# Kernel optimization log

Hardware: AMD Instinct MI355X
Metric: run time of the kernel (lower is better)

Reference implementation:

```python
import jax, jax.numpy as jnp
import numpy as np

# __init__ constants
COORS_RANGE = ((-51.2, 51.2), (-51.2, 51.2), (-4.0, 2.4))  # x, y, z ranges
SPATIAL = (512, 512, 64)  # base spatial shape (X, Y, Z)
SCALES = (2, 4, 8, 1)     # scale_list + [1]
N_POINTS = 2_000_000
N_BATCH = 8


def setup_inputs() -> dict:
    key = jax.random.key(0)
    kp, kb = jax.random.split(key)
    lo = jnp.array([r[0] for r in COORS_RANGE], dtype=jnp.float32)
    hi = jnp.array([r[1] for r in COORS_RANGE], dtype=jnp.float32)
    u = jax.random.uniform(kp, (N_POINTS, 3), dtype=jnp.float32)
    points = lo + u * (hi - lo)  # [N,3] xyz inside the voxelization range
    batch_idx = jax.random.randint(kb, (N_POINTS,), 0, N_BATCH).astype(jnp.int64)
    return {"points": points, "batch_idx": batch_idx}


def reference(points, batch_idx):
    """Per scale: quantize xyz to voxel indices, then unique/dedup with inverse and
    counts. Rows [b,x,y,z] are packed into a single int64 key so that a 1-D unique
    (lexicographically equivalent to torch.unique(dim=0)) can be used.
    Returns, for each scale in SCALES: (full_coors [N,4] int64, coors_inv [N] int,
    coors [M,4] int32 in [b,z,y,x] order), flattened into one tuple."""
    b = batch_idx.astype(jnp.int64)
    outs = []
    for scale in SCALES:
        dims = [int(np.ceil(s / scale)) for s in SPATIAL]  # per-scale grid size
        idxs = []
        for i in range(3):
            lo, hi = COORS_RANGE[i]
            # torch .long() truncates toward zero; values are >=0 in range so
            # truncation == floor here.
            idxs.append((dims[i] * (points[:, i] - lo) / (hi - lo)).astype(jnp.int64))
        xidx, yidx, zidx = idxs
        full_coors = jnp.stack([b, xidx, yidx, zidx], axis=-1)  # [N,4]
        sx, sy, sz = dims
        # pack (b,x,y,z) lexicographically into one key
        keys = ((b * sx + xidx) * sy + yidx) * sz + zidx
        unq, unq_inv, unq_cnt = jnp.unique(keys, return_inverse=True, return_counts=True)
        zb = unq % sz
        rem = unq // sz
        yb = rem % sy
        rem = rem // sy
        xb = rem % sx
        bb = rem // sx
        # original reorders unq columns to [b, z, y, x] and casts to int32
        coors = jnp.stack([bb, zb, yb, xb], axis=-1).astype(jnp.int32)
        outs.extend([full_coors, unq_inv.reshape(-1), coors])
    return tuple(outs)
```

## Files before the change

### kernel.cpp

```cpp
#include <hip/hip_runtime.h>
#include <stdint.h>


#define CHUNK 4096
#define NB    1174
#define TOTALW 4808704
#define R_S2 0
#define R_S4 528384
#define R_S8 598016
#define R_S1 610304
#define PAD0 524288
#define PAD1 593920
#define PAD2 606208
#define PAD3 4804608
#define NBUCKET 512
#define BCAP 5120
#define KEYBLOCKS 1024
#define ROUND 2048
#define KPT 8
#define NB_SMALL 149

__device__ __forceinline__ uint32_t cmp2(uint32_t w) {
  w = (w | (w >> 1)) & 0x55555555u;
  w = (w | (w >> 1)) & 0x33333333u;
  w = (w | (w >> 2)) & 0x0F0F0F0Fu;
  w = (w | (w >> 4)) & 0x00FF00FFu;
  w = (w | (w >> 8)) & 0x0000FFFFu;
  return w;
}

__global__ __launch_bounds__(256) void k_key(
    const float* __restrict__ pts, const int* __restrict__ bidx, int n,
    uint32_t* __restrict__ keys,
    uint32_t* __restrict__ bucketCount, uint32_t* __restrict__ bucketData,
    uint32_t* __restrict__ chunkSums) {
  __shared__ uint32_t cnt[NBUCKET], inc[NBUCKET], pos[NBUCKET], gpos[NBUCKET];
  __shared__ uint32_t shs[256];
  __shared__ uint32_t scratch[ROUND];
  int t = threadIdx.x;
  int base = blockIdx.x * ROUND;

  if (blockIdx.x == 0) {
    if (t < 149) chunkSums[t] = 0;
    if (t == 149) chunkSums[1173] = 0;
  }

  cnt[t] = 0; cnt[t + 256] = 0;
  pos[t] = 0; pos[t + 256] = 0;
  __syncthreads();

  uint32_t myKey[KPT];
  int myBk[KPT];
#pragma unroll
  for (int k = 0; k < KPT; k++) {
    int j = base + k * 256 + t;
    myBk[k] = -1;
    if (j < n) {
      float px = pts[3 * j + 0];
      float py = pts[3 * j + 1];
      float pz = pts[3 * j + 2];
      int b = bidx[j];
      int x1 = (int)((512.0f * (px + 51.2f)) / 102.4f);
      int y1 = (int)((512.0f * (py + 51.2f)) / 102.4f);
      int z1 = (int)((64.0f * (pz + 4.0f)) / 6.4f);
      keys[j] = ((uint32_t)b << 27) | ((uint32_t)x1 << 17) | ((uint32_t)y1 << 7) | (uint32_t)z1;
      uint32_t s1k = (uint32_t)(((b * 512 + x1) * 512 + y1) * 64 + z1);
      if (s1k < (1u << 27)) {
        int bk = (int)(s1k >> 18);
        myBk[k] = bk;
        myKey[k] = s1k;
        atomicAdd(&cnt[bk], 1u);
      }
    }
  }
  __syncthreads();

  uint32_t c0 = cnt[2 * t], c1 = cnt[2 * t + 1];
  gpos[2 * t] = c0 ? atomicAdd(&bucketCount[2 * t], c0) : 0u;
  gpos[2 * t + 1] = c1 ? atomicAdd(&bucketCount[2 * t + 1], c1) : 0u;
  uint32_t s = c0 + c1;
  shs[t] = s;
  __syncthreads();
  for (int off = 1; off < 256; off <<= 1) {
    uint32_t add = (t >= off) ? shs[t - off] : 0u;
    __syncthreads();
    shs[t] += add;
    __syncthreads();
  }
  inc[2 * t] = shs[t] - s + c0;
  inc[2 * t + 1] = shs[t];
  __syncthreads();
  uint32_t total = shs[255];

#pragma unroll
  for (int k = 0; k < KPT; k++) {
    if (myBk[k] >= 0) {
      int bk = myBk[k];
      uint32_t slot = inc[bk] - cnt[bk] + atomicAdd(&pos[bk], 1u);
      scratch[slot] = myKey[k];
    }
  }
  __syncthreads();

#pragma unroll
  for (int m = 0; m < KPT; m++) {
    uint32_t p = (uint32_t)(m * 256 + t);
    if (p < total) {
      uint32_t kk = scratch[p];
      int lo = (int)(kk >> 18);
      uint32_t lidx = p - (inc[lo] - cnt[lo]);
      uint32_t g = gpos[lo] + lidx;
      if (g < BCAP) bucketData[(size_t)lo * BCAP + g] = kk;
    }
  }
}

__device__ __forceinline__ uint32_t blockReduce(uint32_t v, uint32_t* shR, int t) {
  shR[t] = v;
  __syncthreads();
  for (int off = 128; off > 0; off >>= 1) {
    if (t < off) shR[t] += shR[t + off];
    __syncthreads();
  }
  uint32_t r = shR[0];
  __syncthreads();
  return r;
}

__global__ __launch_bounds__(256) void k_bucket(
    const uint32_t* __restrict__ bucketCount, const uint32_t* __restrict__ bucketData,
    uint32_t* __restrict__ bitmap, uint32_t* __restrict__ chunkSums,
    uint2* __restrict__ pairs) {
  __shared__ uint32_t s1L[8192];
  __shared__ uint32_t s2L[1024];
  __shared__ uint32_t s4L[128];
  __shared__ uint32_t shR[256];
  int bk = blockIdx.x, t = threadIdx.x;

  uint4 z4 = make_uint4(0, 0, 0, 0);
  for (int i = t; i < 2048; i += 256) ((uint4*)s1L)[i] = z4;

  if (bk < 3) {
    const int pads[3] = {PAD0, PAD1, PAD2};
    uint4* pz = (uint4*)(bitmap + pads[bk]);
    for (int i = t; i < 1024; i += 256) pz[i] = z4;
  } else if (bk == 3) {
    uint4* pz = (uint4*)(pairs + PAD3);
    for (int i = t; i < 2048; i += 256) pz[i] = z4;
  }
  __syncthreads();

  uint32_t c = bucketCount[bk];
  if (c > BCAP) c = BCAP;
  const uint32_t* src = bucketData + (size_t)bk * BCAP;
  for (uint32_t i = t; i < c; i += 256) {
    uint32_t key = src[i];
    uint32_t local = key & 0x3FFFFu;
    atomicOr(&s1L[local >> 5], 1u << (local & 31u));
  }
  __syncthreads();

  uint32_t wsum = 0;
#pragma unroll
  for (int m = 0; m < 8; m++) {
    uint4 v = ((uint4*)s1L)[8 * t + m];
    wsum += __popc(v.x) + __popc(v.y) + __popc(v.z) + __popc(v.w);
  }
  shR[t] = wsum;
  __syncthreads();
  for (int off = 1; off < 256; off <<= 1) {
    uint32_t add = (t >= off) ? shR[t - off] : 0u;
    __syncthreads();
    shR[t] += add;
    __syncthreads();
  }
  uint32_t S1a = shR[127];
  uint32_t S1b = shR[255] - S1a;
  uint32_t run = shR[t] - wsum;
  if (t >= 128) run -= S1a;
  __syncthreads();
  {
    uint4* pb = (uint4*)(pairs + (R_S1 + (size_t)bk * 8192));
#pragma unroll
    for (int m = 0; m < 8; m++) {
      uint4 v = ((uint4*)s1L)[8 * t + m];
      uint32_t r0 = run;               uint32_t p0 = __popc(v.x);
      uint32_t r1 = r0 + p0;           uint32_t p1 = __popc(v.y);
      uint32_t r2 = r1 + p1;           uint32_t p2 = __popc(v.z);
      uint32_t r3 = r2 + p2;           run = r3 + __popc(v.w);
      int q = (32 * t + 4 * m) >> 1;
      pb[q + 0] = make_uint4(v.x, r0, v.y, r1);
      pb[q + 1] = make_uint4(v.z, r2, v.w, r3);
    }
  }

  for (int i = t; i < 1024; i += 256) {
    int x2r = i >> 8, Y2 = i & 255;
    int a = (2 * x2r * 512 + 2 * Y2) * 2;
    int b2 = ((2 * x2r + 1) * 512 + 2 * Y2) * 2;
    uint32_t Ax = s1L[a], Ay = s1L[a + 1], Az = s1L[a + 2], Aw = s1L[a + 3];
    uint32_t Bx = s1L[b2], By = s1L[b2 + 1], Bz = s1L[b2 + 2], Bw = s1L[b2 + 3];
    s2L[i] = cmp2(Ax | Az | Bx | Bz) | (cmp2(Ay | Aw | By | Bw) << 16);
  }
  __syncthreads();
  uint32_t pc2 = 0;
  for (int i = t; i < 1024; i += 256) {
    uint32_t v = s2L[i];
    bitmap[R_S2 + (size_t)bk * 1024 + i] = v;
    pc2 += __popc(v);
  }

  uint32_t pc4 = 0;
  if (t < 128) {
    int x4r = t >> 6, kk = t & 63;
    int a = (2 * x4r) * 256 + 4 * kk;
    int b4 = (2 * x4r + 1) * 256 + 4 * kk;
    uint32_t A0 = s2L[a], A1 = s2L[a + 1], A2 = s2L[a + 2], A3 = s2L[a + 3];
    uint32_t B0 = s2L[b4], B1 = s2L[b4 + 1], B2 = s2L[b4 + 2], B3 = s2L[b4 + 3];
    uint32_t v = cmp2(A0 | A1 | B0 | B1) | (cmp2(A2 | A3 | B2 | B3) << 16);
    s4L[t] = v;
    pc4 = __popc(v);
  }
  __syncthreads();
  if (t < 128) bitmap[R_S4 + (size_t)bk * 128 + t] = s4L[t];

  uint32_t pc8 = 0;
  if (t < 16) {
    uint32_t res = 0;
#pragma unroll
    for (int j = 0; j < 4; j++) {
      uint32_t u = s4L[4 * t + j] | s4L[64 + 4 * t + j];
      u = (u | (u >> 16)) & 0xFFFFu;
      res |= cmp2(u) << (8 * j);
    }
    bitmap[R_S8 + (size_t)bk * 16 + t] = res;
    pc8 = __popc(res);
  }

  uint32_t S2 = blockReduce(pc2, shR, t);
  uint32_t S4 = blockReduce(pc4, shR, t);
  uint32_t S8 = blockReduce(pc8, shR, t);
  if (t == 0) {
    chunkSums[149 + 2 * bk] = S1a;
    chunkSums[150 + 2 * bk] = S1b;
    atomicAdd(&chunkSums[bk >> 2], S2);
    atomicAdd(&chunkSums[129 + (bk >> 5)], S4);
    atomicAdd(&chunkSums[146 + (bk >> 8)], S8);
  }
}

__global__ __launch_bounds__(256) void k_scanB(
    uint32_t* blockSums, long long* devOff, uint32_t* devRank, long long fiveN) {
  __shared__ uint32_t sh[256];
  __shared__ uint32_t shB[3];
  int t = threadIdx.x;
  uint32_t v[8];
  uint32_t s = 0;
#pragma unroll
  for (int k = 0; k < 8; k++) {
    int idx = t * 8 + k;
    uint32_t x = (idx < NB) ? blockSums[idx] : 0u;
    v[k] = x;
    s += x;
  }
  sh[t] = s;
  __syncthreads();
  for (int off = 1; off < 256; off <<= 1) {
    uint32_t add = (t >= off) ? sh[t - off] : 0u;
    __syncthreads();
    sh[t] += add;
    __syncthreads();
  }
  uint32_t run = sh[t] - s;
#pragma unroll
  for (int k = 0; k < 8; k++) {
    int idx = t * 8 + k;
    if (idx < NB) blockSums[idx] = run;
    if (idx == 129) shB[0] = run;
    if (idx == 146) shB[1] = run;
    if (idx == 149) shB[2] = run;
    run += v[k];
  }
  __syncthreads();
  if (t == 0) {
    uint32_t tot = sh[255];
    uint32_t T0 = shB[0];
    uint32_t T1 = shB[1] - shB[0];
    uint32_t T2 = shB[2] - shB[1];
    uint32_t T3 = tot - shB[2];
    devOff[0] = 0;
    devOff[1] = devOff[0] + fiveN + 4LL * T0;
    devOff[2] = devOff[1] + fiveN + 4LL * T1;
    devOff[3] = devOff[2] + fiveN + 4LL * T2;
    devOff[4] = devOff[3] + fiveN + 4LL * T3;
    devRank[0] = 0;
    devRank[1] = shB[0];
    devRank[2] = shB[1];
    devRank[3] = shB[2];
  }
}

__global__ __launch_bounds__(256) void k_pref(
    const uint32_t* __restrict__ bitmap, const uint32_t* __restrict__ blockSums,
    uint2* __restrict__ pairs) {
  __shared__ uint32_t sh[256];
  int t = threadIdx.x;
  size_t w0 = (size_t)blockIdx.x * CHUNK + t * 16;
  const uint4* bp = (const uint4*)(bitmap + w0);
  uint4 words[4];
  uint32_t s = 0;
#pragma unroll
  for (int k = 0; k < 4; k++) {
    uint4 v = bp[k];
    words[k] = v;
    s += __popc(v.x) + __popc(v.y) + __popc(v.z) + __popc(v.w);
  }
  sh[t] = s;
  __syncthreads();
  for (int off = 1; off < 256; off <<= 1) {
    uint32_t add = (t >= off) ? sh[t - off] : 0u;
    __syncthreads();
    sh[t] += add;
    __syncthreads();
  }
  uint32_t run = blockSums[blockIdx.x] + (sh[t] - s);
  uint4* pp = (uint4*)(pairs + w0);
#pragma unroll
  for (int k = 0; k < 4; k++) {
    uint4 o1, o2;
    o1.x = words[k].x; o1.y = run; run += __popc(words[k].x);
    o1.z = words[k].y; o1.w = run; run += __popc(words[k].y);
    o2.x = words[k].z; o2.y = run; run += __popc(words[k].z);
    o2.z = words[k].w; o2.w = run; run += __popc(words[k].w);
    pp[2 * k] = o1;
    pp[2 * k + 1] = o2;
  }
}

template <int LZ, int LYZ, int LB, int MZ, int MY, int MX, int RG, int SCALE_IDX>
__device__ __forceinline__ void uniq_region(
    uint32_t w, uint32_t wd, uint32_t pf, uint32_t rankBase,
    const long long* __restrict__ devOff, int* __restrict__ out, long long fiveN) {
  uint32_t pos = pf - rankBase;
  long long base = devOff[SCALE_IDX] + fiveN;
  uint32_t local = w - (uint32_t)RG;
  while (wd) {
    int bit = __ffs(wd) - 1;
    wd &= wd - 1u;
    uint32_t key = (local << 5) + (uint32_t)bit;
    int z = (int)(key & (uint32_t)MZ);
    int y = (int)((key >> LZ) & (uint32_t)MY);
    int x = (int)((key >> LYZ) & (uint32_t)MX);
    int bb = (int)(key >> LB);
    *(int4*)(out + base + 4LL * pos) = make_int4(bb, z, y, x);
    pos++;
  }
}

__global__ __launch_bounds__(256) void k_out(
    const uint32_t* __restrict__ keys, int n, const uint2* __restrict__ pairs,
    const uint32_t* __restrict__ devRank, const long long* __restrict__ devOff,
    const uint32_t* __restrict__ cs, int* __restrict__ out,
    long long fourN, long long fiveN, int NW) {
  int bid = blockIdx.x;
  int t = threadIdx.x;
  if (bid < 4 * NW) {
    int sec = bid / NW;
    int wb = bid - sec * NW;
    if (sec == 0) {
      long long o = devOff[3];
      uint32_t rnk = devRank[3];
#pragma unroll
      for (int half = 0; half < 2; half++) {
        int j = wb * 512 + half * 256 + t;
        if (j >= n) continue;
        uint32_t p = keys[j];
        int b = (int)(p >> 27);
        int x1 = (int)((p >> 17) & 1023u);
        int y1 = (int)((p >> 7) & 1023u);
        int z1 = (int)(p & 127u);
        uint32_t key = (uint32_t)(((b * 512 + x1) * 512 + y1) * 64 + z1);
        uint2 pr = pairs[R_S1 + (key >> 5)];
        *(int4*)(out + o + 4LL * j) = make_int4(b, x1, y1, z1);
        uint32_t inv = cs[149 + (key >> 17)] + pr.y +
                       __popc(pr.x & ((1u << (key & 31u)) - 1u)) - rnk;
        out[o + fourN + j] = (int)inv;
      }
    } else {
      int i = sec - 1;
      const int SX[3] = {256, 128, 64};
      const int SZ[3] = {32, 16, 8};
      const int SH[3] = {1, 2, 3};
      const int RG[3] = {R_S2, R_S4, R_S8};
      int sh = SH[i], sx = SX[i], sz = SZ[i], rg = RG[i];
      long long o = devOff[i];
      uint32_t rnk = devRank[i];
#pragma unroll
      for (int half = 0; half < 2; half++) {
        int j = wb * 512 + half * 256 + t;
        if (j >= n) continue;
        uint32_t p = keys[j];
        int b = (int)(p >> 27);
        int x1 = (int)((p >> 17) & 1023u);
        int y1 = (int)((p >> 7) & 1023u);
        int z1 = (int)(p & 127u);
        int xi = x1 >> sh, yi = y1 >> sh, zi = z1 >> sh;
        uint32_t key = (uint32_t)(((b * sx + xi) * sx + yi) * sz + zi);
        uint2 pr = pairs[rg + (key >> 5)];
        *(int4*)(out + o + 4LL * j) = make_int4(b, xi, yi, zi);
        uint32_t inv = pr.y + __popc(pr.x & ((1u << (key & 31u)) - 1u)) - rnk;
        out[o + fourN + j] = (int)inv;
      }
    }
  } else {
    uint32_t w = (uint32_t)(bid - 4 * NW) * 256 + t;
    uint2 pr = pairs[w];
    if (!pr.x) return;
    if (w < R_S4) {
      uniq_region<5, 13, 21, 31, 255, 255, R_S2, 0>(w, pr.x, pr.y, devRank[0], devOff, out, fiveN);
    } else if (w < R_S8) {
      uniq_region<4, 11, 18, 15, 127, 127, R_S4, 1>(w, pr.x, pr.y, devRank[1], devOff, out, fiveN);
    } else if (w < R_S1) {
      uniq_region<3, 9, 15, 7, 63, 63, R_S8, 2>(w, pr.x, pr.y, devRank[2], devOff, out, fiveN);
    } else {
      uniq_region<6, 15, 24, 63, 511, 511, R_S1, 3>(
          w, pr.x, pr.y + cs[w >> 12], devRank[3], devOff, out, fiveN);
    }
  }
}

extern "C" void kernel_launch(void* const* d_in, const int* in_sizes, int n_in,
                              void* d_out, int out_size, void* d_ws, size_t ws_size,
                              hipStream_t stream) {
  const float* pts = (const float*)d_in[0];
  const int* bidx = (const int*)d_in[1];
  int n = in_sizes[0] / 3;
  int* out = (int*)d_out;

  char* ws = (char*)d_ws;
  long long* devOff = (long long*)ws;
  uint32_t* devRank = (uint32_t*)(ws + 64);
  uint32_t* chunkSums = (uint32_t*)(ws + 256);
  uint32_t* bucketCount = (uint32_t*)(ws + 5120);
  uint32_t* bitmap = (uint32_t*)(ws + 8192);
  uint2* pairs = (uint2*)(ws + 19243008);
  uint32_t* keys = (uint32_t*)(ws + 57712640);
  uint32_t* bucketData = (uint32_t*)(ws + 65712640);

  const long long fourN = 4LL * n, fiveN = 5LL * n;
  const int NW = (n + 511) / 512;

  hipMemsetAsync(bucketCount, 0, NBUCKET * 4, stream);
  hipLaunchKernelGGL(k_key, dim3(KEYBLOCKS), dim3(256), 0, stream,
                     pts, bidx, n, keys, bucketCount, bucketData, chunkSums);
  hipLaunchKernelGGL(k_bucket, dim3(NBUCKET), dim3(256), 0, stream,
                     bucketCount, bucketData, bitmap, chunkSums, pairs);
  hipLaunchKernelGGL(k_scanB, dim3(1), dim3(256), 0, stream, chunkSums, devOff, devRank, fiveN);
  hipLaunchKernelGGL(k_pref, dim3(NB_SMALL), dim3(256), 0, stream, bitmap, chunkSums, pairs);
  hipLaunchKernelGGL(k_out, dim3(4 * NW + TOTALW / 256), dim3(256), 0, stream,
                     keys, n, pairs, devRank, devOff, chunkSums, out, fourN, fiveN, NW);
}
```

Measured before the change: 427.4 us.

## Fuse coarse-scale prefix computation into bucket kernel and drop k_pref pass

The bucket kernel now computes per-bucket exclusive prefix counts for the 2x, 4x and 8x coarse bitmaps and writes (word, prefix) pairs directly. The separate bitmap buffer and the k_pref kernel go away, and a single-block scan produces per-bucket bases that k_out adds on lookup. This removes one kernel launch plus a bitmap write and re-read. In exchange, k_bucket runs extra block-wide scans with many syncthreads, and k_out does one more global load per inverse index.

Result: no change. 422.6 us (median of 2 runs) (-1.1%).

```diff
diff --git a/kernel.cpp b/kernel.cpp
--- a/kernel.cpp
+++ b/kernel.cpp
@@ -2,8 +2,6 @@
 #include <stdint.h>
 
 
-#define CHUNK 4096
-#define NB    1174
 #define TOTALW 4808704
 #define R_S2 0
 #define R_S4 528384
@@ -15,10 +13,10 @@
 #define PAD3 4804608
 #define NBUCKET 512
 #define BCAP 5120
+#define NSUM 2560
 #define KEYBLOCKS 1024
 #define ROUND 2048
 #define KPT 8
-#define NB_SMALL 149
 
 __device__ __forceinline__ uint32_t cmp2(uint32_t w) {
   w = (w | (w >> 1)) & 0x55555555u;
@@ -29,21 +27,28 @@
   return w;
 }
 
+__device__ __forceinline__ uint32_t scan256(uint32_t v, uint32_t* shR, int t) {
+  __syncthreads();
+  shR[t] = v;
+  __syncthreads();
+  for (int off = 1; off < 256; off <<= 1) {
+    uint32_t add = (t >= off) ? shR[t - off] : 0u;
+    __syncthreads();
+    shR[t] += add;
+    __syncthreads();
+  }
+  return shR[t];
+}
+
 __global__ __launch_bounds__(256) void k_key(
     const float* __restrict__ pts, const int* __restrict__ bidx, int n,
     uint32_t* __restrict__ keys,
-    uint32_t* __restrict__ bucketCount, uint32_t* __restrict__ bucketData,
-    uint32_t* __restrict__ chunkSums) {
+    uint32_t* __restrict__ bucketCount, uint32_t* __restrict__ bucketData) {
   __shared__ uint32_t cnt[NBUCKET], inc[NBUCKET], pos[NBUCKET], gpos[NBUCKET];
   __shared__ uint32_t shs[256];
   __shared__ uint32_t scratch[ROUND];
   int t = threadIdx.x;
   int base = blockIdx.x * ROUND;
-
-  if (blockIdx.x == 0) {
-    if (t < 149) chunkSums[t] = 0;
-    if (t == 149) chunkSums[1173] = 0;
-  }
 
   cnt[t] = 0; cnt[t + 256] = 0;
   pos[t] = 0; pos[t + 256] = 0;
@@ -115,22 +120,9 @@
   }
 }
 
-__device__ __forceinline__ uint32_t blockReduce(uint32_t v, uint32_t* shR, int t) {
-  shR[t] = v;
-  __syncthreads();
-  for (int off = 128; off > 0; off >>= 1) {
-    if (t < off) shR[t] += shR[t + off];
-    __syncthreads();
-  }
-  uint32_t r = shR[0];
-  __syncthreads();
-  return r;
-}
-
 __global__ __launch_bounds__(256) void k_bucket(
     const uint32_t* __restrict__ bucketCount, const uint32_t* __restrict__ bucketData,
-    uint32_t* __restrict__ bitmap, uint32_t* __restrict__ chunkSums,
-    uint2* __restrict__ pairs) {
+    uint32_t* __restrict__ sums, uint2* __restrict__ pairs) {
   __shared__ uint32_t s1L[8192];
   __shared__ uint32_t s2L[1024];
   __shared__ uint32_t s4L[128];
@@ -140,12 +132,9 @@
   uint4 z4 = make_uint4(0, 0, 0, 0);
   for (int i = t; i < 2048; i += 256) ((uint4*)s1L)[i] = z4;
 
-  if (bk < 3) {
-    const int pads[3] = {PAD0, PAD1, PAD2};
-    uint4* pz = (uint4*)(bitmap + pads[bk]);
-    for (int i = t; i < 1024; i += 256) pz[i] = z4;
-  } else if (bk == 3) {
-    uint4* pz = (uint4*)(pairs + PAD3);
+  if (bk < 4) {
+    const int pads[4] = {PAD0, PAD1, PAD2, PAD3};
+    uint4* pz = (uint4*)(pairs + pads[bk]);
     for (int i = t; i < 2048; i += 256) pz[i] = z4;
   }
   __syncthreads();
@@ -166,19 +155,11 @@
     uint4 v = ((uint4*)s1L)[8 * t + m];
     wsum += __popc(v.x) + __popc(v.y) + __popc(v.z) + __popc(v.w);
   }
-  shR[t] = wsum;
-  __syncthreads();
-  for (int off = 1; off < 256; off <<= 1) {
-    uint32_t add = (t >= off) ? shR[t - off] : 0u;
-    __syncthreads();
-    shR[t] += add;
-    __syncthreads();
-  }
+  uint32_t incl1 = scan256(wsum, shR, t);
   uint32_t S1a = shR[127];
-  uint32_t S1b = shR[255] - S1a;
-  uint32_t run = shR[t] - wsum;
+  uint32_t S1tot = shR[255];
+  uint32_t run = incl1 - wsum;
   if (t >= 128) run -= S1a;
-  __syncthreads();
   {
     uint4* pb = (uint4*)(pairs + (R_S1 + (size_t)bk * 8192));
 #pragma unroll
@@ -203,63 +184,70 @@
     s2L[i] = cmp2(Ax | Az | Bx | Bz) | (cmp2(Ay | Aw | By | Bw) << 16);
   }
   __syncthreads();
-  uint32_t pc2 = 0;
-  for (int i = t; i < 1024; i += 256) {
-    uint32_t v = s2L[i];
-    bitmap[R_S2 + (size_t)bk * 1024 + i] = v;
-    pc2 += __popc(v);
-  }
-
-  uint32_t pc4 = 0;
+  uint32_t a0 = s2L[4 * t], a1 = s2L[4 * t + 1], a2 = s2L[4 * t + 2], a3 = s2L[4 * t + 3];
+  uint32_t sum2 = __popc(a0) + __popc(a1) + __popc(a2) + __popc(a3);
+  uint32_t incl2 = scan256(sum2, shR, t);
+  uint32_t S2tot = shR[255];
+  uint32_t run2 = incl2 - sum2;
+  {
+    uint4* pb = (uint4*)(pairs + (R_S2 + (size_t)bk * 1024));
+    uint32_t r1 = run2 + __popc(a0);
+    uint32_t r2 = r1 + __popc(a1);
+    uint32_t r3 = r2 + __popc(a2);
+    pb[2 * t + 0] = make_uint4(a0, run2, a1, r1);
+    pb[2 * t + 1] = make_uint4(a2, r2, a3, r3);
+  }
+
+  uint32_t v4 = 0;
   if (t < 128) {
     int x4r = t >> 6, kk = t & 63;
     int a = (2 * x4r) * 256 + 4 * kk;
     int b4 = (2 * x4r + 1) * 256 + 4 * kk;
     uint32_t A0 = s2L[a], A1 = s2L[a + 1], A2 = s2L[a + 2], A3 = s2L[a + 3];
     uint32_t B0 = s2L[b4], B1 = s2L[b4 + 1], B2 = s2L[b4 + 2], B3 = s2L[b4 + 3];
-    uint32_t v = cmp2(A0 | A1 | B0 | B1) | (cmp2(A2 | A3 | B2 | B3) << 16);
-    s4L[t] = v;
-    pc4 = __popc(v);
-  }
-  __syncthreads();
-  if (t < 128) bitmap[R_S4 + (size_t)bk * 128 + t] = s4L[t];
-
-  uint32_t pc8 = 0;
+    v4 = cmp2(A0 | A1 | B0 | B1) | (cmp2(A2 | A3 | B2 | B3) << 16);
+    s4L[t] = v4;
+  }
+  uint32_t incl4 = scan256(__popc(v4), shR, t);
+  uint32_t S4tot = shR[255];
+  uint32_t run4 = incl4 - __popc(v4);
+  if (t < 128) pairs[R_S4 + (size_t)bk * 128 + t] = make_uint2(v4, run4);
+
+  uint32_t v8 = 0;
   if (t < 16) {
-    uint32_t res = 0;
 #pragma unroll
     for (int j = 0; j < 4; j++) {
       uint32_t u = s4L[4 * t + j] | s4L[64 + 4 * t + j];
       u = (u | (u >> 16)) & 0xFFFFu;
-      res |= cmp2(u) << (8 * j);
-    }
-    bitmap[R_S8 + (size_t)bk * 16 + t] = res;
-    pc8 = __popc(res);
-  }
-
-  uint32_t S2 = blockReduce(pc2, shR, t);
-  uint32_t S4 = blockReduce(pc4, shR, t);
-  uint32_t S8 = blockReduce(pc8, shR, t);
+      v8 |= cmp2(u) << (8 * j);
+    }
+  }
+  uint32_t incl8 = scan256(__popc(v8), shR, t);
+  uint32_t S8tot = shR[255];
+  uint32_t run8 = incl8 - __popc(v8);
+  if (t < 16) pairs[R_S8 + (size_t)bk * 16 + t] = make_uint2(v8, run8);
+
   if (t == 0) {
-    chunkSums[149 + 2 * bk] = S1a;
-    chunkSums[150 + 2 * bk] = S1b;
-    atomicAdd(&chunkSums[bk >> 2], S2);
-    atomicAdd(&chunkSums[129 + (bk >> 5)], S4);
-    atomicAdd(&chunkSums[146 + (bk >> 8)], S8);
+    sums[bk] = S2tot;
+    sums[512 + bk] = S4tot;
+    sums[1024 + bk] = S8tot;
+    sums[1536 + 2 * bk] = S1a;
+    sums[1537 + 2 * bk] = S1tot - S1a;
   }
 }
 
 __global__ __launch_bounds__(256) void k_scanB(
-    uint32_t* blockSums, long long* devOff, uint32_t* devRank, long long fiveN) {
+    const uint32_t* __restrict__ sums, uint32_t* __restrict__ bases,
+    long long* __restrict__ devOff, long long fiveN) {
   __shared__ uint32_t sh[256];
   __shared__ uint32_t shB[3];
   int t = threadIdx.x;
-  uint32_t v[8];
+  uint32_t v[10];
   uint32_t s = 0;
 #pragma unroll
-  for (int k = 0; k < 8; k++) {
-    int idx = t * 8 + k;
-    uint32_t x = (idx < NB) ? blockSums[idx] : 0u;
+  for (int k = 0; k < 10; k++) {
+    int idx = t * 10 + k;
+    uint32_t x = sums[idx];
     v[k] = x;
     s += x;
   }
@@ -273,75 +261,42 @@
   }
   uint32_t run = sh[t] - s;
 #pragma unroll
-  for (int k = 0; k < 8; k++) {
-    int idx = t * 8 + k;
-    if (idx < NB) blockSums[idx] = run;
-    if (idx == 129) shB[0] = run;
-    if (idx == 146) shB[1] = run;
-    if (idx == 149) shB[2] = run;
+  for (int k = 0; k < 10; k++) {
+    int idx = t * 10 + k;
+    if (idx == 512) shB[0] = run;
+    if (idx == 1024) shB[1] = run;
+    if (idx == 1536) shB[2] = run;
     run += v[k];
   }
   __syncthreads();
+  uint32_t B0 = shB[0], B1 = shB[1], B2 = shB[2];
+  run = sh[t] - s;
+#pragma unroll
+  for (int k = 0; k < 10; k++) {
+    int idx = t * 10 + k;
+    uint32_t sub = (idx < 512) ? 0u : (idx < 1024) ? B0 : (idx < 1536) ? B1 : B2;
+    bases[idx] = run - sub;
+    run += v[k];
+  }
   if (t == 0) {
     uint32_t tot = sh[255];
-    uint32_t T0 = shB[0];
-    uint32_t T1 = shB[1] - shB[0];
-    uint32_t T2 = shB[2] - shB[1];
-    uint32_t T3 = tot - shB[2];
+    uint32_t T0 = B0;
+    uint32_t T1 = B1 - B0;
+    uint32_t T2 = B2 - B1;
+    uint32_t T3 = tot - B2;
     devOff[0] = 0;
     devOff[1] = devOff[0] + fiveN + 4LL * T0;
     devOff[2] = devOff[1] + fiveN + 4LL * T1;
     devOff[3] = devOff[2] + fiveN + 4LL * T2;
     devOff[4] = devOff[3] + fiveN + 4LL * T3;
-    devRank[0] = 0;
-    devRank[1] = shB[0];
-    devRank[2] = shB[1];
-    devRank[3] = shB[2];
-  }
-}
-
-__global__ __launch_bounds__(256) void k_pref(
-    const uint32_t* __restrict__ bitmap, const uint32_t* __restrict__ blockSums,
-    uint2* __restrict__ pairs) {
-  __shared__ uint32_t sh[256];
-  int t = threadIdx.x;
-  size_t w0 = (size_t)blockIdx.x * CHUNK + t * 16;
-  const uint4* bp = (const uint4*)(bitmap + w0);
-  uint4 words[4];
-  uint32_t s = 0;
-#pragma unroll
-  for (int k = 0; k < 4; k++) {
-    uint4 v = bp[k];
-    words[k] = v;
-    s += __popc(v.x) + __popc(v.y) + __popc(v.z) + __popc(v.w);
-  }
-  sh[t] = s;
-  __syncthreads();
-  for (int off = 1; off < 256; off <<= 1) {
-    uint32_t add = (t >= off) ? sh[t - off] : 0u;
-    __syncthreads();
-    sh[t] += add;
-    __syncthreads();
-  }
-  uint32_t run = blockSums[blockIdx.x] + (sh[t] - s);
-  uint4* pp = (uint4*)(pairs + w0);
-#pragma unroll
-  for (int k = 0; k < 4; k++) {
-    uint4 o1, o2;
-    o1.x = words[k].x; o1.y = run; run += __popc(words[k].x);
-    o1.z = words[k].y; o1.w = run; run += __popc(words[k].y);
-    o2.x = words[k].z; o2.y = run; run += __popc(words[k].z);
-    o2.z = words[k].w; o2.w = run; run += __popc(words[k].w);
-    pp[2 * k] = o1;
-    pp[2 * k + 1] = o2;
   }
 }
 
 template <int LZ, int LYZ, int LB, int MZ, int MY, int MX, int RG, int SCALE_IDX>
 __device__ __forceinline__ void uniq_region(
-    uint32_t w, uint32_t wd, uint32_t pf, uint32_t rankBase,
+    uint32_t w, uint32_t wd, uint32_t pf,
     const long long* __restrict__ devOff, int* __restrict__ out, long long fiveN) {
-  uint32_t pos = pf - rankBase;
+  uint32_t pos = pf;
   long long base = devOff[SCALE_IDX] + fiveN;
   uint32_t local = w - (uint32_t)RG;
   while (wd) {
@@ -359,9 +314,8 @@
 
 __global__ __launch_bounds__(256) void k_out(
     const uint32_t* __restrict__ keys, int n, const uint2* __restrict__ pairs,
-    const uint32_t* __restrict__ devRank, const long long* __restrict__ devOff,
-    const uint32_t* __restrict__ cs, int* __restrict__ out,
-    long long fourN, long long fiveN, int NW) {
+    const uint32_t* __restrict__ bs, const long long* __restrict__ devOff,
+    int* __restrict__ out, long long fourN, long long fiveN, int NW) {
   int bid = blockIdx.x;
   int t = threadIdx.x;
   if (bid < 4 * NW) {
@@ -369,7 +323,6 @@
     int wb = bid - sec * NW;
     if (sec == 0) {
       long long o = devOff[3];
-      uint32_t rnk = devRank[3];
 #pragma unroll
       for (int half = 0; half < 2; half++) {
         int j = wb * 512 + half * 256 + t;
@@ -382,8 +335,8 @@
         uint32_t key = (uint32_t)(((b * 512 + x1) * 512 + y1) * 64 + z1);
         uint2 pr = pairs[R_S1 + (key >> 5)];
         *(int4*)(out + o + 4LL * j) = make_int4(b, x1, y1, z1);
-        uint32_t inv = cs[149 + (key >> 17)] + pr.y +
-                       __popc(pr.x & ((1u << (key & 31u)) - 1u)) - rnk;
+        uint32_t inv = bs[1536 + (key >> 17)] + pr.y +
+                       __popc(pr.x & ((1u << (key & 31u)) - 1u));
         out[o + fourN + j] = (int)inv;
       }
     } else {
@@ -392,9 +345,10 @@
       const int SZ[3] = {32, 16, 8};
       const int SH[3] = {1, 2, 3};
       const int RG[3] = {R_S2, R_S4, R_S8};
+      const int BO[3] = {0, 512, 1024};
+      const int BS[3] = {15, 12, 9};
       int sh = SH[i], sx = SX[i], sz = SZ[i], rg = RG[i];
       long long o = devOff[i];
-      uint32_t rnk = devRank[i];
 #pragma unroll
       for (int half = 0; half < 2; half++) {
         int j = wb * 512 + half * 256 + t;
@@ -408,7 +362,8 @@
         uint32_t key = (uint32_t)(((b * sx + xi) * sx + yi) * sz + zi);
         uint2 pr = pairs[rg + (key >> 5)];
         *(int4*)(out + o + 4LL * j) = make_int4(b, xi, yi, zi);
-        uint32_t inv = pr.y + __popc(pr.x & ((1u << (key & 31u)) - 1u)) - rnk;
+        uint32_t inv = bs[BO[i] + (key >> BS[i])] + pr.y +
+                       __popc(pr.x & ((1u << (key & 31u)) - 1u));
         out[o + fourN + j] = (int)inv;
       }
     }
@@ -417,14 +372,17 @@
     uint2 pr = pairs[w];
     if (!pr.x) return;
     if (w < R_S4) {
-      uniq_region<5, 13, 21, 31, 255, 255, R_S2, 0>(w, pr.x, pr.y, devRank[0], devOff, out, fiveN);
+      uniq_region<5, 13, 21, 31, 255, 255, R_S2, 0>(
+          w, pr.x, pr.y + bs[w >> 10], devOff, out, fiveN);
     } else if (w < R_S8) {
-      uniq_region<4, 11, 18, 15, 127, 127, R_S4, 1>(w, pr.x, pr.y, devRank[1], devOff, out, fiveN);
+      uniq_region<4, 11, 18, 15, 127, 127, R_S4, 1>(
+          w, pr.x, pr.y + bs[512 + ((w - R_S4) >> 7)], devOff, out, fiveN);
     } else if (w < R_S1) {
-      uniq_region<3, 9, 15, 7, 63, 63, R_S8, 2>(w, pr.x, pr.y, devRank[2], devOff, out, fiveN);
+      uniq_region<3, 9, 15, 7, 63, 63, R_S8, 2>(
+          w, pr.x, pr.y + bs[1024 + ((w - R_S8) >> 4)], devOff, out, fiveN);
     } else {
       uniq_region<6, 15, 24, 63, 511, 511, R_S1, 3>(
-          w, pr.x, pr.y + cs[w >> 12], devRank[3], devOff, out, fiveN);
+          w, pr.x, pr.y + bs[1536 + ((w - R_S1) >> 12)], devOff, out, fiveN);
     }
   }
 }
@@ -439,10 +397,9 @@
 
   char* ws = (char*)d_ws;
   long long* devOff = (long long*)ws;
-  uint32_t* devRank = (uint32_t*)(ws + 64);
-  uint32_t* chunkSums = (uint32_t*)(ws + 256);
-  uint32_t* bucketCount = (uint32_t*)(ws + 5120);
-  uint32_t* bitmap = (uint32_t*)(ws + 8192);
+  uint32_t* sums = (uint32_t*)(ws + 256);
+  uint32_t* bases = (uint32_t*)(ws + 12288);
+  uint32_t* bucketCount = (uint32_t*)(ws + 24576);
   uint2* pairs = (uint2*)(ws + 19243008);
   uint32_t* keys = (uint32_t*)(ws + 57712640);
   uint32_t* bucketData = (uint32_t*)(ws + 65712640);
@@ -452,11 +409,11 @@
 
   hipMemsetAsync(bucketCount, 0, NBUCKET * 4, stream);
   hipLaunchKernelGGL(k_key, dim3(KEYBLOCKS), dim3(256), 0, stream,
-                     pts, bidx, n, keys, bucketCount, bucketData, chunkSums);
+                     pts, bidx, n, keys, bucketCount, bucketData);
   hipLaunchKernelGGL(k_bucket, dim3(NBUCKET), dim3(256), 0, stream,
-                     bucketCount, bucketData, bitmap, chunkSums, pairs);
-  hipLaunchKernelGGL(k_scanB, dim3(1), dim3(256), 0, stream, chunkSums, devOff, devRank, fiveN);
-  hipLaunchKernelGGL(k_pref, dim3(NB_SMALL), dim3(256), 0, stream, bitmap, chunkSums, pairs);
+                     bucketCount, bucketData, sums, pairs);
+  hipLaunchKernelGGL(k_scanB, dim3(1), dim3(256), 0, stream,
+                     sums, bases, devOff, fiveN);
   hipLaunchKernelGGL(k_out, dim3(4 * NW + TOTALW / 256), dim3(256), 0, stream,
-                     keys, n, pairs, devRank, devOff, chunkSums, out, fourN, fiveN, NW);
-}
+                     keys, n, pairs, bases, devOff, out, fourN, fiveN, NW);
+}
```
